# Optimization experiments

Measured on AMD Instinct MI355X. Metric: run time of the kernel, lower is better.

Reference implementation:

```python
import jax, jax.numpy as jnp
import numpy as np

B, N, D = 4, 4096, 768
H, DH = 12, 64          # heads, dim_head; inner_dim = H*DH = D
DEPTH = 4
HID = int(D * 4.0)      # mlp hidden
LN_EPS = 1e-5


def setup_inputs() -> dict:
    key = jax.random.key(0)
    ks = jax.random.split(key, 7)
    s = 0.02
    return {
        "x": jax.random.normal(ks[0], (B, N, D), jnp.float32),
        "ln1_g": jnp.ones((DEPTH, D), jnp.float32),
        "ln1_b": jnp.zeros((DEPTH, D), jnp.float32),
        "qkv_w": jax.random.normal(ks[1], (DEPTH, D, H * DH), jnp.float32) * s,
        "temp": jnp.ones((DEPTH, H, 1), jnp.float32),
        "out_w": jax.random.normal(ks[2], (DEPTH, H * DH, D), jnp.float32) * s,
        "out_b": jnp.zeros((DEPTH, D), jnp.float32),
        "ln2_g": jnp.ones((DEPTH, D), jnp.float32),
        "ln2_b": jnp.zeros((DEPTH, D), jnp.float32),
        "fc1_w": jax.random.normal(ks[3], (DEPTH, D, HID), jnp.float32) * s,
        "fc1_b": jnp.zeros((DEPTH, HID), jnp.float32),
        "fc2_w": jax.random.normal(ks[4], (DEPTH, HID, D), jnp.float32) * s,
        "fc2_b": jnp.zeros((DEPTH, D), jnp.float32),
    }


def _layernorm(x, g, b):
    mu = jnp.mean(x, axis=-1, keepdims=True)
    var = jnp.mean((x - mu) ** 2, axis=-1, keepdims=True)
    return (x - mu) * jax.lax.rsqrt(var + LN_EPS) * g + b


def _tss_attention(h, qkv_w, temp, out_w, out_b):
    b, n, d = h.shape
    w = h @ qkv_w                                   # (b, n, H*DH)
    w = w.reshape(b, n, H, DH).transpose(0, 2, 1, 3)  # (b, h, n, d)
    # F.normalize over token dim (dim=-2), eps=1e-12
    nrm = jnp.sqrt(jnp.sum(w * w, axis=2, keepdims=True))
    w_normed = w / jnp.maximum(nrm, 1e-12)
    logits = jnp.sum(w_normed * w_normed, axis=-1) * temp[None]  # (b, h, n)
    Pi = jax.nn.softmax(logits, axis=-1)
    Pi_n = Pi / (jnp.sum(Pi, axis=-1, keepdims=True) + 1e-8)
    dots = jnp.einsum('bhn,bhnd->bhd', Pi_n, w * w)[:, :, None, :]  # (b, h, 1, d)
    attn = 1.0 / (1.0 + dots)
    out = -(w * Pi[..., None]) * attn               # (b, h, n, d)
    out = out.transpose(0, 2, 1, 3).reshape(b, n, H * DH)
    return out @ out_w + out_b


def reference(x, ln1_g, ln1_b, qkv_w, temp, out_w, out_b,
              ln2_g, ln2_b, fc1_w, fc1_b, fc2_w, fc2_b):
    for i in range(DEPTH):
        h = _layernorm(x, ln1_g[i], ln1_b[i])
        x = _tss_attention(h, qkv_w[i], temp[i], out_w[i], out_b[i]) + x
        h2 = _layernorm(x, ln2_g[i], ln2_b[i])
        mlp = jax.nn.gelu(h2 @ fc1_w[i] + fc1_b[i], approximate=False) @ fc2_w[i] + fc2_b[i]
        x = mlp + x
    return x
```

## Files before the change

### kernel.cpp

```cpp
#include <hip/hip_runtime.h>
#include <cstdint>
#include <cstddef>

static constexpr int Bc = 4, Nc = 4096, Dc = 768, Hc = 12, DHc = 64;
static constexpr int HIDc = 3072, DEPTHc = 4;
static constexpr int Mc = Bc * Nc;
static constexpr int BHc = Bc * Hc;
static constexpr int BHDc = BHc * DHc;

typedef unsigned short u16;
typedef __bf16 bf16x8 __attribute__((ext_vector_type(8)));
typedef float  f32x4  __attribute__((ext_vector_type(4)));

#define DEV __device__ __forceinline__

DEV u16 f2bf(float x) {
    uint32_t u = __float_as_uint(x);
    u += 0x7fffu + ((u >> 16) & 1u);
    return (u16)(u >> 16);
}
DEV float bf2f(u16 u) { return __uint_as_float(((uint32_t)u) << 16); }
DEV void unp2(uint32_t u, float& a, float& b) {
    a = __uint_as_float(u << 16);
    b = __uint_as_float(u & 0xffff0000u);
}
DEV float gelu_fast(float x) {
    float y = 0.7978845608f * (x + 0.044715f * x * x * x);
    float e = __expf(2.0f * y);
    float t = 1.0f - 2.0f / (e + 1.0f);
    return 0.5f * x * (1.0f + t);
}

DEV void ldg_lds16(const void* g, void* l) {
    __builtin_amdgcn_global_load_lds(
        (const __attribute__((address_space(1))) uint32_t*)(uintptr_t)g,
        (__attribute__((address_space(3))) uint32_t*)(uint32_t)(uintptr_t)l,
        16, 0, 0);
}

__global__ void detect_kernel(const uint32_t* __restrict__ x, uint32_t* __restrict__ flag) {
    int t = threadIdx.x;
    uint32_t w = x[t];
    int e = (w >> 7) & 0xFF;
    __shared__ int cnt[256];
    cnt[t] = (e >= 100 && e <= 140) ? 1 : 0;
    __syncthreads();
    for (int s = 128; s; s >>= 1) {
        if (t < s) cnt[t] += cnt[t + s];
        __syncthreads();
    }
    if (t == 0) flag[0] = (cnt[0] >= 128) ? 1u : 0u;
}

__global__ __launch_bounds__(256) void sentinel_kernel(u16* __restrict__ out, int n) {
    int i = blockIdx.x * 256 + threadIdx.x;
    if (i < n) out[i] = 0x449A;
}

__global__ __launch_bounds__(256) void cvt_param_kernel(
    const void* __restrict__ src, float* __restrict__ dst, int n,
    const uint32_t* __restrict__ flag) {
    int i = blockIdx.x * 256 + threadIdx.x;
    if (i >= n) return;
    if (flag[0]) dst[i] = bf2f(((const u16*)src)[i]);
    else         dst[i] = ((const float*)src)[i];
}

__global__ __launch_bounds__(256) void transpose_cvt_off(
    const void* __restrict__ src, size_t eoff, u16* __restrict__ dst,
    int R, int C, const uint32_t* __restrict__ flag) {
    __shared__ u16 tile[32][33];
    const bool isbf = (flag[0] != 0);
    int c0 = blockIdx.x * 32, r0 = blockIdx.y * 32;
    int tx = threadIdx.x & 31, ty = threadIdx.x >> 5;
#pragma unroll
    for (int j = 0; j < 32; j += 8) {
        size_t off = eoff + (size_t)(r0 + ty + j) * C + (c0 + tx);
        tile[ty + j][tx] = isbf ? ((const u16*)src)[off] : f2bf(((const float*)src)[off]);
    }
    __syncthreads();
#pragma unroll
    for (int j = 0; j < 32; j += 8)
        dst[(size_t)(c0 + ty + j) * R + (r0 + tx)] = tile[tx][ty + j];
}

__global__ __launch_bounds__(256) void ln_kernel(
    const float* __restrict__ x, const float* __restrict__ g,
    const float* __restrict__ bta, u16* __restrict__ out) {
    int row = blockIdx.x, t = threadIdx.x;
    const float* xr = x + (size_t)row * Dc;
    float v0 = xr[t], v1 = xr[t + 256], v2 = xr[t + 512];
    float s = v0 + v1 + v2;
    float ss = v0 * v0 + v1 * v1 + v2 * v2;
    __shared__ float red[8];
    for (int m = 32; m; m >>= 1) { s += __shfl_xor(s, m, 64); ss += __shfl_xor(ss, m, 64); }
    int wave = t >> 6, lane = t & 63;
    if (lane == 0) { red[wave] = s; red[4 + wave] = ss; }
    __syncthreads();
    s  = red[0] + red[1] + red[2] + red[3];
    ss = red[4] + red[5] + red[6] + red[7];
    float mu = s * (1.0f / Dc);
    float var = ss * (1.0f / Dc) - mu * mu;
    float rs = rsqrtf(var + 1e-5f);
    u16* orow = out + (size_t)row * Dc;
    orow[t]       = f2bf((v0 - mu) * rs * g[t]       + bta[t]);
    orow[t + 256] = f2bf((v1 - mu) * rs * g[t + 256] + bta[t + 256]);
    orow[t + 512] = f2bf((v2 - mu) * rs * g[t + 512] + bta[t + 512]);
}

template <int MODE>
__global__ __launch_bounds__(512, 2) void gemm_kernel(
    const u16* __restrict__ A, const u16* __restrict__ Bt,
    float* Cf, u16* Cb, const float* __restrict__ bias, const float* res,
    float* aux, int M, int N, int K) {
    __shared__ __attribute__((aligned(16))) u16 lds[4][2][256 * 32];
    const int tid = threadIdx.x;
    const int wave = tid >> 6, lane = tid & 63;
    const int wm = wave >> 2, wn = wave & 3;
    const int bm = blockIdx.y * 256, bn = blockIdx.x * 256;
    const int NT = K >> 5;

    const int srow   = lane >> 2;
    const int schunk = (lane & 3) ^ ((lane >> 3) & 3);
    const u16* ag = A  + (size_t)(bm + wave * 16 + srow) * K + schunk * 8;
    const u16* bg = Bt + (size_t)(bn + wave * 16 + srow) * K + schunk * 8;
    const size_t rstep = (size_t)128 * K;

    auto stA = [&](int t) {
        u16* d = &lds[t & 3][0][wave * 512];
        const u16* g = ag + (size_t)t * 32;
        ldg_lds16(g, d);
        ldg_lds16(g + rstep, d + 4096);
    };
    auto stB = [&](int t) {
        u16* d = &lds[t & 3][1][wave * 512];
        const u16* g = bg + (size_t)t * 32;
        ldg_lds16(g, d);
        ldg_lds16(g + rstep, d + 4096);
    };

    const int fm = lane & 15;
    const int fc = lane >> 4;
    const int fp = fc ^ ((fm >> 1) & 3);
    const int aoff = (wm * 128 + fm) * 32 + fp * 8;
    const int boff = (wn * 64  + fm) * 32 + fp * 8;

    f32x4 acc[8][4] = {};

    stA(0); stB(0); stA(1); stB(1);
    asm volatile("s_waitcnt vmcnt(4)" ::: "memory");
    __builtin_amdgcn_s_barrier();
    __builtin_amdgcn_sched_barrier(0);

    for (int t = 0; t < NT; ++t) {
        const int tb = t & 3;
        const u16* Ab = &lds[tb][0][0];
        const u16* Bb = &lds[tb][1][0];
        bf16x8 af[8], bq[4];
#pragma unroll
        for (int mf = 0; mf < 8; ++mf)
            af[mf] = *(const bf16x8*)(Ab + aoff + mf * 512);
        bq[0] = *(const bf16x8*)(Bb + boff);
        bq[1] = *(const bf16x8*)(Bb + boff + 512);
        if (t + 2 < NT) stA(t + 2);
        __builtin_amdgcn_s_barrier();
        __builtin_amdgcn_sched_barrier(0);
        __builtin_amdgcn_s_setprio(1);
#pragma unroll
        for (int mf = 0; mf < 8; ++mf) {
            acc[mf][0] = __builtin_amdgcn_mfma_f32_16x16x32_bf16(af[mf], bq[0], acc[mf][0], 0, 0, 0);
            acc[mf][1] = __builtin_amdgcn_mfma_f32_16x16x32_bf16(af[mf], bq[1], acc[mf][1], 0, 0, 0);
        }
        __builtin_amdgcn_s_setprio(0);
        __builtin_amdgcn_s_barrier();
        __builtin_amdgcn_sched_barrier(0);
        bq[2] = *(const bf16x8*)(Bb + boff + 1024);
        bq[3] = *(const bf16x8*)(Bb + boff + 1536);
        if (t + 2 < NT) {
            stB(t + 2);
            asm volatile("s_waitcnt vmcnt(4)" ::: "memory");
        } else if (t + 1 < NT) {
            asm volatile("s_waitcnt vmcnt(0)" ::: "memory");
        }
        __builtin_amdgcn_s_barrier();
        __builtin_amdgcn_sched_barrier(0);
        __builtin_amdgcn_s_setprio(1);
#pragma unroll
        for (int mf = 0; mf < 8; ++mf) {
            acc[mf][2] = __builtin_amdgcn_mfma_f32_16x16x32_bf16(af[mf], bq[2], acc[mf][2], 0, 0, 0);
            acc[mf][3] = __builtin_amdgcn_mfma_f32_16x16x32_bf16(af[mf], bq[3], acc[mf][3], 0, 0, 0);
        }
        __builtin_amdgcn_s_setprio(0);
        __builtin_amdgcn_s_barrier();
        __builtin_amdgcn_sched_barrier(0);
    }

    const int er = (lane >> 4) * 4;
    const int ec = lane & 15;
    float csq[4] = {0.f, 0.f, 0.f, 0.f};
#pragma unroll
    for (int mf = 0; mf < 8; ++mf) {
        const int row0 = bm + wm * 128 + mf * 16 + er;
#pragma unroll
        for (int nf = 0; nf < 4; ++nf) {
            const int col = bn + wn * 64 + nf * 16 + ec;
#pragma unroll
            for (int r = 0; r < 4; ++r) {
                const size_t off = (size_t)(row0 + r) * N + col;
                float v = acc[mf][nf][r];
                if (MODE == 1) {
                    Cf[off] = v + bias[col] + res[off];
                } else if (MODE == 2) {
                    Cb[off] = f2bf(gelu_fast(v + bias[col]));
                } else {
                    Cb[off] = f2bf(v);
                    csq[nf] += v * v;
                }
            }
        }
    }
    if (MODE == 3) {
        const int b = bm >> 12;
#pragma unroll
        for (int nf = 0; nf < 4; ++nf) {
            float s = csq[nf];
            s += __shfl_xor(s, 16, 64);
            s += __shfl_xor(s, 32, 64);
            if (lane < 16) {
                const int col = bn + wn * 64 + nf * 16 + lane;
                const int bh = b * Hc + (col >> 6);
                atomicAdd(&aux[bh * DHc + (col & 63)], s);
            }
        }
    }
}

__global__ __launch_bounds__(256) void logits_kernel(
    const u16* __restrict__ w, const float* __restrict__ nrm2,
    const float* __restrict__ tp, float* __restrict__ logits) {
    int blk = blockIdx.x;
    int chunk = blk & 15, bh = blk >> 4;
    int b = bh / Hc, h = bh - b * Hc;
    int t = threadIdx.x, dq = t & 3, nr = t >> 2;
    __shared__ float inv[64];
    if (t < 64) inv[t] = 1.0f / fmaxf(nrm2[bh * DHc + t], 1e-24f);
    __syncthreads();
    float tl = tp[h];
#pragma unroll
    for (int jj = 0; jj < 4; jj++) {
        int n = chunk * 256 + jj * 64 + nr;
        const uint4* wr = (const uint4*)(w + ((size_t)b * Nc + n) * Dc + h * DHc + dq * 16);
        uint4 u0 = wr[0], u1 = wr[1];
        float acc = 0.f;
        float e0, e1;
        const float* iv = inv + dq * 16;
        unp2(u0.x, e0, e1); acc += e0 * e0 * iv[0]  + e1 * e1 * iv[1];
        unp2(u0.y, e0, e1); acc += e0 * e0 * iv[2]  + e1 * e1 * iv[3];
        unp2(u0.z, e0, e1); acc += e0 * e0 * iv[4]  + e1 * e1 * iv[5];
        unp2(u0.w, e0, e1); acc += e0 * e0 * iv[6]  + e1 * e1 * iv[7];
        unp2(u1.x, e0, e1); acc += e0 * e0 * iv[8]  + e1 * e1 * iv[9];
        unp2(u1.y, e0, e1); acc += e0 * e0 * iv[10] + e1 * e1 * iv[11];
        unp2(u1.z, e0, e1); acc += e0 * e0 * iv[12] + e1 * e1 * iv[13];
        unp2(u1.w, e0, e1); acc += e0 * e0 * iv[14] + e1 * e1 * iv[15];
        acc += __shfl_xor(acc, 1, 64);
        acc += __shfl_xor(acc, 2, 64);
        if (dq == 0) logits[(size_t)bh * Nc + n] = tl * acc;
    }
}

__global__ __launch_bounds__(256) void softmax_kernel(
    const float* __restrict__ logits, float* __restrict__ Pi, float* __restrict__ rowsc) {
    int bh = blockIdx.x, t = threadIdx.x;
    int wave = t >> 6, lane = t & 63;
    const float4* lg = (const float4*)(logits + (size_t)bh * Nc);
    float4 v[4];
    float mx = -3.4e38f;
    __shared__ float red[4];
#pragma unroll
    for (int j = 0; j < 4; j++) {
        v[j] = lg[t + 256 * j];
        mx = fmaxf(mx, fmaxf(fmaxf(v[j].x, v[j].y), fmaxf(v[j].z, v[j].w)));
    }
    for (int m = 32; m; m >>= 1) mx = fmaxf(mx, __shfl_xor(mx, m, 64));
    if (lane == 0) red[wave] = mx;
    __syncthreads();
    mx = fmaxf(fmaxf(red[0], red[1]), fmaxf(red[2], red[3]));
    __syncthreads();
    float s = 0.f;
#pragma unroll
    for (int j = 0; j < 4; j++) {
        v[j].x = expf(v[j].x - mx); v[j].y = expf(v[j].y - mx);
        v[j].z = expf(v[j].z - mx); v[j].w = expf(v[j].w - mx);
        s += v[j].x + v[j].y + v[j].z + v[j].w;
    }
    for (int m = 32; m; m >>= 1) s += __shfl_xor(s, m, 64);
    if (lane == 0) red[wave] = s;
    __syncthreads();
    s = red[0] + red[1] + red[2] + red[3];
    __syncthreads();
    float invs = 1.0f / s;
    float s2 = 0.f;
    float4* Pr = (float4*)(Pi + (size_t)bh * Nc);
#pragma unroll
    for (int j = 0; j < 4; j++) {
        float4 p;
        p.x = v[j].x * invs; p.y = v[j].y * invs;
        p.z = v[j].z * invs; p.w = v[j].w * invs;
        s2 += p.x + p.y + p.z + p.w;
        Pr[t + 256 * j] = p;
    }
    for (int m = 32; m; m >>= 1) s2 += __shfl_xor(s2, m, 64);
    if (lane == 0) red[wave] = s2;
    __syncthreads();
    if (t == 0) rowsc[bh] = 1.0f / (red[0] + red[1] + red[2] + red[3] + 1e-8f);
}

__global__ __launch_bounds__(256) void dots_kernel(
    const u16* __restrict__ w, const float* __restrict__ Pi,
    const float* __restrict__ rowsc, float* __restrict__ dots) {
    int blk = blockIdx.x;
    int chunk = blk & 15, bh = blk >> 4;
    int b = bh / Hc, h = bh - b * Hc;
    int t = threadIdx.x, d4 = t & 15, rg = t >> 4;
    const u16* base = w + ((size_t)b * Nc + chunk * 256 + rg) * Dc + h * DHc + d4 * 4;
    const float* Prow = Pi + (size_t)bh * Nc + chunk * 256 + rg;
    float4 acc = {0.f, 0.f, 0.f, 0.f};
#pragma unroll 4
    for (int j = 0; j < 16; j++) {
        uint2 u = *(const uint2*)(base + (size_t)j * 16 * Dc);
        float p = Prow[j * 16];
        float a0, a1, a2, a3;
        unp2(u.x, a0, a1); unp2(u.y, a2, a3);
        acc.x += p * a0 * a0; acc.y += p * a1 * a1;
        acc.z += p * a2 * a2; acc.w += p * a3 * a3;
    }
    __shared__ float4 red[256];
    red[t] = acc;
    __syncthreads();
    if (t < 64) {
        float s = 0.f;
#pragma unroll
        for (int r = 0; r < 16; r++) {
            const float* f = (const float*)&red[r * 16 + (t >> 2)];
            s += f[t & 3];
        }
        atomicAdd(&dots[bh * DHc + t], s * rowsc[bh]);
    }
}

__global__ __launch_bounds__(256) void attnout_kernel(
    const u16* __restrict__ w, const float* __restrict__ Pi,
    const float* __restrict__ dots, u16* __restrict__ out) {
    int idx = blockIdx.x * 256 + threadIdx.x;
    int cg = idx % (Dc / 8);
    int m = idx / (Dc / 8);
    int b = m >> 12, n = m & 4095;
    int c = cg * 8, h = c >> 6, d = c & 63;
    int bh = b * Hc + h;
    uint4 wv = ((const uint4*)w)[idx];
    float pi = Pi[(size_t)bh * Nc + n];
    float4 dv0 = *(const float4*)(dots + bh * DHc + d);
    float4 dv1 = *(const float4*)(dots + bh * DHc + d + 4);
    float a0, a1, a2, a3, a4, a5, a6, a7;
    unp2(wv.x, a0, a1); unp2(wv.y, a2, a3);
    unp2(wv.z, a4, a5); unp2(wv.w, a6, a7);
    union { u16 u[8]; uint4 v4; } pk;
    pk.u[0] = f2bf(-(a0 * pi) / (1.0f + dv0.x));
    pk.u[1] = f2bf(-(a1 * pi) / (1.0f + dv0.y));
    pk.u[2] = f2bf(-(a2 * pi) / (1.0f + dv0.z));
    pk.u[3] = f2bf(-(a3 * pi) / (1.0f + dv0.w));
    pk.u[4] = f2bf(-(a4 * pi) / (1.0f + dv1.x));
    pk.u[5] = f2bf(-(a5 * pi) / (1.0f + dv1.y));
    pk.u[6] = f2bf(-(a6 * pi) / (1.0f + dv1.z));
    pk.u[7] = f2bf(-(a7 * pi) / (1.0f + dv1.w));
    ((uint4*)out)[idx] = pk.v4;
}

extern "C" void kernel_launch(void* const* d_in, const int* in_sizes, int n_in,
                              void* d_out, int out_size, void* d_ws, size_t ws_size,
                              hipStream_t stream) {
    const void* x_in = d_in[0];
    const void* ln1g = d_in[1];
    const void* ln1b = d_in[2];
    const void* qkvw = d_in[3];
    const void* temp = d_in[4];
    const void* outw = d_in[5];
    const void* outb = d_in[6];
    const void* ln2g = d_in[7];
    const void* ln2b = d_in[8];
    const void* fc1w = d_in[9];
    const void* fc1b = d_in[10];
    const void* fc2w = d_in[11];
    const void* fc2b = d_in[12];

    char* p = (char*)d_ws;
    auto alloc = [&](size_t bytes) {
        void* r = (void*)p;
        p += (bytes + 255) & ~(size_t)255;
        return r;
    };
    float* xbuf = (float*)alloc((size_t)Mc * Dc * 4);
    void*  big  = alloc((size_t)Mc * HIDc * 2);
    u16*   wbuf = (u16*)big;
    u16*   gbuf = (u16*)big;
    u16*  abuf  = (u16*)alloc((size_t)Mc * Dc * 2);
    const size_t QKV_T = (size_t)Dc * Dc, OUT_T = (size_t)Dc * Dc;
    const size_t FC1_T = (size_t)HIDc * Dc, FC2_T = (size_t)Dc * HIDc;
    const size_t LSTRIDE = QKV_T + OUT_T + FC1_T + FC2_T;
    u16*  wTL   = (u16*)alloc(LSTRIDE * 2);
    float* nrm2 = (float*)alloc((size_t)BHDc * 4);
    float* dots = (float*)alloc((size_t)BHDc * 4);
    float* logit = (float*)alloc((size_t)BHc * Nc * 4);
    float* Pi    = (float*)alloc((size_t)BHc * Nc * 4);
    float* rowsc = (float*)alloc((size_t)BHc * 4);
    uint32_t* flag = (uint32_t*)alloc(256);
    float* ln1g_f = (float*)alloc((size_t)DEPTHc * Dc * 4);
    float* ln1b_f = (float*)alloc((size_t)DEPTHc * Dc * 4);
    float* ln2g_f = (float*)alloc((size_t)DEPTHc * Dc * 4);
    float* ln2b_f = (float*)alloc((size_t)DEPTHc * Dc * 4);
    float* outb_f = (float*)alloc((size_t)DEPTHc * Dc * 4);
    float* fc1b_f = (float*)alloc((size_t)DEPTHc * HIDc * 4);
    float* fc2b_f = (float*)alloc((size_t)DEPTHc * Dc * 4);
    float* temp_f = (float*)alloc((size_t)DEPTHc * Hc * 4);
    if ((size_t)(p - (char*)d_ws) > ws_size) {
        sentinel_kernel<<<(out_size + 255) / 256, 256, 0, stream>>>((u16*)d_out, out_size);
        return;
    }

    detect_kernel<<<1, 256, 0, stream>>>((const uint32_t*)x_in, flag);

    auto cvt = [&](const void* s, float* d, int n) {
        cvt_param_kernel<<<(n + 255) / 256, 256, 0, stream>>>(s, d, n, flag);
    };
    cvt(x_in, xbuf, Mc * Dc);
    cvt(ln1g, ln1g_f, DEPTHc * Dc);
    cvt(ln1b, ln1b_f, DEPTHc * Dc);
    cvt(ln2g, ln2g_f, DEPTHc * Dc);
    cvt(ln2b, ln2b_f, DEPTHc * Dc);
    cvt(outb, outb_f, DEPTHc * Dc);
    cvt(fc1b, fc1b_f, DEPTHc * HIDc);
    cvt(fc2b, fc2b_f, DEPTHc * Dc);
    cvt(temp, temp_f, DEPTHc * Hc);

    u16* qkvT = wTL;
    u16* outT = qkvT + QKV_T;
    u16* fc1T = outT + OUT_T;
    u16* fc2T = fc1T + FC1_T;

    for (int i = 0; i < DEPTHc; i++) {
        transpose_cvt_off<<<dim3(Dc / 32, Dc / 32), 256, 0, stream>>>(
            qkvw, (size_t)i * Dc * Dc, qkvT, Dc, Dc, flag);
        transpose_cvt_off<<<dim3(Dc / 32, Dc / 32), 256, 0, stream>>>(
            outw, (size_t)i * Dc * Dc, outT, Dc, Dc, flag);
        transpose_cvt_off<<<dim3(HIDc / 32, Dc / 32), 256, 0, stream>>>(
            fc1w, (size_t)i * Dc * HIDc, fc1T, Dc, HIDc, flag);
        transpose_cvt_off<<<dim3(Dc / 32, HIDc / 32), 256, 0, stream>>>(
            fc2w, (size_t)i * HIDc * Dc, fc2T, HIDc, Dc, flag);

        ln_kernel<<<Mc, 256, 0, stream>>>(xbuf, ln1g_f + i * Dc, ln1b_f + i * Dc, abuf);
        hipMemsetAsync(nrm2, 0, (size_t)2 * BHDc * 4, stream);
        gemm_kernel<3><<<dim3(Dc / 256, Mc / 256), 512, 0, stream>>>(
            abuf, qkvT, nullptr, wbuf, nullptr, nullptr, nrm2, Mc, Dc, Dc);
        logits_kernel<<<BHc * 16, 256, 0, stream>>>(wbuf, nrm2, temp_f + i * Hc, logit);
        softmax_kernel<<<BHc, 256, 0, stream>>>(logit, Pi, rowsc);
        dots_kernel<<<BHc * 16, 256, 0, stream>>>(wbuf, Pi, rowsc, dots);
        attnout_kernel<<<(Mc * Dc / 8) / 256, 256, 0, stream>>>(wbuf, Pi, dots, abuf);
        gemm_kernel<1><<<dim3(Dc / 256, Mc / 256), 512, 0, stream>>>(
            abuf, outT, xbuf, nullptr, outb_f + i * Dc, xbuf, nullptr, Mc, Dc, Dc);
        ln_kernel<<<Mc, 256, 0, stream>>>(xbuf, ln2g_f + i * Dc, ln2b_f + i * Dc, abuf);
        gemm_kernel<2><<<dim3(HIDc / 256, Mc / 256), 512, 0, stream>>>(
            abuf, fc1T, nullptr, gbuf, fc1b_f + i * HIDc, nullptr, nullptr, Mc, HIDc, Dc);
        gemm_kernel<1><<<dim3(Dc / 256, Mc / 256), 512, 0, stream>>>(
            gbuf, fc2T, xbuf, nullptr, fc2b_f + i * Dc, xbuf, nullptr, Mc, Dc, HIDc);
    }
    hipMemcpyAsync(d_out, xbuf, (size_t)Mc * Dc * 4, hipMemcpyDeviceToDevice, stream);
}
```

Before: 1.709 ms.

## Restructure GEMM main loop with register double-buffered A fragments and deeper prefetch

```diff
diff --git a/kernel.cpp b/kernel.cpp
--- a/kernel.cpp
+++ b/kernel.cpp
@@ -126,19 +126,6 @@
     const u16* bg = Bt + (size_t)(bn + wave * 16 + srow) * K + schunk * 8;
     const size_t rstep = (size_t)128 * K;
 
-    auto stA = [&](int t) {
-        u16* d = &lds[t & 3][0][wave * 512];
-        const u16* g = ag + (size_t)t * 32;
-        ldg_lds16(g, d);
-        ldg_lds16(g + rstep, d + 4096);
-    };
-    auto stB = [&](int t) {
-        u16* d = &lds[t & 3][1][wave * 512];
-        const u16* g = bg + (size_t)t * 32;
-        ldg_lds16(g, d);
-        ldg_lds16(g + rstep, d + 4096);
-    };
-
     const int fm = lane & 15;
     const int fc = lane >> 4;
     const int fp = fc ^ ((fm >> 1) & 3);
@@ -146,54 +133,66 @@
     const int boff = (wn * 64  + fm) * 32 + fp * 8;
 
     f32x4 acc[8][4] = {};
-
-    stA(0); stB(0); stA(1); stB(1);
+    bf16x8 af0[8], af1[8];
+
+#define GEMM_STAGE(T)                                                       \
+    {   const int tt_ = (T); const int sc_ = (tt_ < NT) ? tt_ : 0;          \
+        const int sl_ = tt_ & 3;                                            \
+        u16* dA_ = &lds[sl_][0][wave * 512];                                \
+        u16* dB_ = &lds[sl_][1][wave * 512];                                \
+        const u16* gA_ = ag + (size_t)sc_ * 32;                             \
+        const u16* gB_ = bg + (size_t)sc_ * 32;                             \
+        ldg_lds16(gA_, dA_); ldg_lds16(gA_ + rstep, dA_ + 4096);            \
+        ldg_lds16(gB_, dB_); ldg_lds16(gB_ + rstep, dB_ + 4096); }
+
+#define GEMM_ITER(H, CUR, NXT)                                              \
+    {                                                                       \
+        asm volatile("s_waitcnt vmcnt(4)" ::: "memory");                    \
+        __builtin_amdgcn_s_barrier();                                       \
+        __builtin_amdgcn_sched_barrier(0);                                  \
+        GEMM_STAGE((H) + 3);                                                \
+        bf16x8 bq0, bq1, bq2, bq3;                                          \
+        {   const u16* Bb_ = &lds[(H) & 3][1][0];                           \
+            bq0 = *(const bf16x8*)(Bb_ + boff);                             \
+            bq1 = *(const bf16x8*)(Bb_ + boff + 512);                       \
+            bq2 = *(const bf16x8*)(Bb_ + boff + 1024);                      \
+            bq3 = *(const bf16x8*)(Bb_ + boff + 1536); }                    \
+        __builtin_amdgcn_sched_barrier(0);                                  \
+        {   const u16* Ab_ = &lds[((H) + 1) & 3][0][0];                     \
+            _Pragma("unroll")                                               \
+            for (int mf = 0; mf < 8; ++mf)                                  \
+                NXT[mf] = *(const bf16x8*)(Ab_ + aoff + mf * 512); }        \
+        asm volatile("s_waitcnt lgkmcnt(8)" ::: "memory");                  \
+        __builtin_amdgcn_sched_barrier(0);                                  \
+        __builtin_amdgcn_s_setprio(1);                                      \
+        _Pragma("unroll")                                                   \
+        for (int mf = 0; mf < 8; ++mf) {                                    \
+            acc[mf][0] = __builtin_amdgcn_mfma_f32_16x16x32_bf16(CUR[mf], bq0, acc[mf][0], 0, 0, 0); \
+            acc[mf][1] = __builtin_amdgcn_mfma_f32_16x16x32_bf16(CUR[mf], bq1, acc[mf][1], 0, 0, 0); \
+            acc[mf][2] = __builtin_amdgcn_mfma_f32_16x16x32_bf16(CUR[mf], bq2, acc[mf][2], 0, 0, 0); \
+            acc[mf][3] = __builtin_amdgcn_mfma_f32_16x16x32_bf16(CUR[mf], bq3, acc[mf][3], 0, 0, 0); \
+        }                                                                   \
+        __builtin_amdgcn_s_setprio(0);                                      \
+    }
+
+    GEMM_STAGE(0);
+    GEMM_STAGE(1);
     asm volatile("s_waitcnt vmcnt(4)" ::: "memory");
     __builtin_amdgcn_s_barrier();
     __builtin_amdgcn_sched_barrier(0);
-
-    for (int t = 0; t < NT; ++t) {
-        const int tb = t & 3;
-        const u16* Ab = &lds[tb][0][0];
-        const u16* Bb = &lds[tb][1][0];
-        bf16x8 af[8], bq[4];
+    {   const u16* Ab_ = &lds[0][0][0];
 #pragma unroll
         for (int mf = 0; mf < 8; ++mf)
-            af[mf] = *(const bf16x8*)(Ab + aoff + mf * 512);
-        bq[0] = *(const bf16x8*)(Bb + boff);
-        bq[1] = *(const bf16x8*)(Bb + boff + 512);
-        if (t + 2 < NT) stA(t + 2);
-        __builtin_amdgcn_s_barrier();
-        __builtin_amdgcn_sched_barrier(0);
-        __builtin_amdgcn_s_setprio(1);
-#pragma unroll
-        for (int mf = 0; mf < 8; ++mf) {
-            acc[mf][0] = __builtin_amdgcn_mfma_f32_16x16x32_bf16(af[mf], bq[0], acc[mf][0], 0, 0, 0);
-            acc[mf][1] = __builtin_amdgcn_mfma_f32_16x16x32_bf16(af[mf], bq[1], acc[mf][1], 0, 0, 0);
-        }
-        __builtin_amdgcn_s_setprio(0);
-        __builtin_amdgcn_s_barrier();
-        __builtin_amdgcn_sched_barrier(0);
-        bq[2] = *(const bf16x8*)(Bb + boff + 1024);
-        bq[3] = *(const bf16x8*)(Bb + boff + 1536);
-        if (t + 2 < NT) {
-            stB(t + 2);
-            asm volatile("s_waitcnt vmcnt(4)" ::: "memory");
-        } else if (t + 1 < NT) {
-            asm volatile("s_waitcnt vmcnt(0)" ::: "memory");
-        }
-        __builtin_amdgcn_s_barrier();
-        __builtin_amdgcn_sched_barrier(0);
-        __builtin_amdgcn_s_setprio(1);
-#pragma unroll
-        for (int mf = 0; mf < 8; ++mf) {
-            acc[mf][2] = __builtin_amdgcn_mfma_f32_16x16x32_bf16(af[mf], bq[2], acc[mf][2], 0, 0, 0);
-            acc[mf][3] = __builtin_amdgcn_mfma_f32_16x16x32_bf16(af[mf], bq[3], acc[mf][3], 0, 0, 0);
-        }
-        __builtin_amdgcn_s_setprio(0);
-        __builtin_amdgcn_s_barrier();
-        __builtin_amdgcn_sched_barrier(0);
-    }
+            af0[mf] = *(const bf16x8*)(Ab_ + aoff + mf * 512);
+    }
+    GEMM_STAGE(2);
+
+    for (int h = 0; h < NT; h += 2) {
+        GEMM_ITER(h,     af0, af1);
+        GEMM_ITER(h + 1, af1, af0);
+    }
+#undef GEMM_ITER
+#undef GEMM_STAGE
 
     const int er = (lane >> 4) * 4;
     const int ec = lane & 15;
```

Result: no change. 1.727 ms (+1.0%).

## Restructure GEMM main loop into 64-wide K stages with ping-pong LDS buffers

Applied to the files above, without the earlier changes.

```diff
diff --git a/kernel.cpp b/kernel.cpp
--- a/kernel.cpp
+++ b/kernel.cpp
@@ -113,87 +113,120 @@
     const u16* __restrict__ A, const u16* __restrict__ Bt,
     float* Cf, u16* Cb, const float* __restrict__ bias, const float* res,
     float* aux, int M, int N, int K) {
-    __shared__ __attribute__((aligned(16))) u16 lds[4][2][256 * 32];
+    __shared__ __attribute__((aligned(16))) u16 lds[2][2][2][256 * 32];
     const int tid = threadIdx.x;
     const int wave = tid >> 6, lane = tid & 63;
     const int wm = wave >> 2, wn = wave & 3;
     const int bm = blockIdx.y * 256, bn = blockIdx.x * 256;
-    const int NT = K >> 5;
-
-    const int srow   = lane >> 2;
+    const int NKS = K >> 6;
+
+    u16* Lm = &lds[0][0][0][0];
+    const u16* L = Lm;
+
     const int schunk = (lane & 3) ^ ((lane >> 3) & 3);
-    const u16* ag = A  + (size_t)(bm + wave * 16 + srow) * K + schunk * 8;
-    const u16* bg = Bt + (size_t)(bn + wave * 16 + srow) * K + schunk * 8;
-    const size_t rstep = (size_t)128 * K;
-
-    auto stA = [&](int t) {
-        u16* d = &lds[t & 3][0][wave * 512];
-        const u16* g = ag + (size_t)t * 32;
-        ldg_lds16(g, d);
-        ldg_lds16(g + rstep, d + 4096);
-    };
-    auto stB = [&](int t) {
-        u16* d = &lds[t & 3][1][wave * 512];
-        const u16* g = bg + (size_t)t * 32;
-        ldg_lds16(g, d);
-        ldg_lds16(g + rstep, d + 4096);
-    };
-
-    const int fm = lane & 15;
-    const int fc = lane >> 4;
-    const int fp = fc ^ ((fm >> 1) & 3);
-    const int aoff = (wm * 128 + fm) * 32 + fp * 8;
-    const int boff = (wn * 64  + fm) * 32 + fp * 8;
+    const u16* ag = A  + (size_t)(bm + wave * 16 + (lane >> 2)) * K + schunk * 8;
+    const u16* bg = Bt + (size_t)(bn + wave * 16 + (lane >> 2)) * K + schunk * 8;
+    const size_t jstep = (size_t)128 * K;
+
+    const int fm = lane & 15, fc = lane >> 4;
+    const int chunk = (fc ^ ((fm >> 1) & 3)) * 8;
+    const int aE0 = (wm * 128 + fm) * 32 + chunk;
+    const int aE1 = 8192 + aE0;
+    const int bE0 = 32768 + (wn * 64 + fm) * 32 + chunk;
+    const int bE1 = 8192 + bE0;
 
     f32x4 acc[8][4] = {};
-
-    stA(0); stB(0); stA(1); stB(1);
+    bf16x8 afr[8], bq[2], bq2[2];
+
+#define STG(OP, GB, SS, DD, KH)                                              \
+    {   const u16* g_ = GB + (size_t)(SS) * 64 + (KH) * 32;                  \
+        u16* d_ = Lm + (OP) * 32768 + (DD) * 16384 + (KH) * 8192 + wave * 512; \
+        ldg_lds16(g_, d_);                                                   \
+        ldg_lds16(g_ + jstep, d_ + 4096); }
+
+#define MF2(NB, BQ)                                                          \
+    __builtin_amdgcn_s_setprio(1);                                           \
+    _Pragma("unroll")                                                        \
+    for (int m = 0; m < 8; ++m) {                                            \
+        acc[m][(NB)]     = __builtin_amdgcn_mfma_f32_16x16x32_bf16(          \
+            afr[m], BQ[0], acc[m][(NB)], 0, 0, 0);                           \
+        acc[m][(NB) + 1] = __builtin_amdgcn_mfma_f32_16x16x32_bf16(          \
+            afr[m], BQ[1], acc[m][(NB) + 1], 0, 0, 0);                       \
+    }                                                                        \
+    __builtin_amdgcn_s_setprio(0);
+
+#define BAR_LG0                                                              \
+    __builtin_amdgcn_s_barrier();                                            \
+    asm volatile("s_waitcnt lgkmcnt(0)" ::: "memory");                       \
+    __builtin_amdgcn_sched_barrier(0);
+
+#define BAR_END                                                              \
+    __builtin_amdgcn_s_barrier();                                            \
+    __builtin_amdgcn_sched_barrier(0);
+
+#define BAR_VM4                                                              \
+    asm volatile("s_waitcnt vmcnt(4)" ::: "memory");                         \
+    __builtin_amdgcn_s_barrier();                                            \
+    __builtin_amdgcn_sched_barrier(0);
+
+#define KSTEP(D, SS1) {                                                      \
+                          \
+    _Pragma("unroll")                                                        \
+    for (int m = 0; m < 8; ++m)                                              \
+        afr[m] = *(const bf16x8*)(L + (D) * 16384 + aE0 + m * 512);          \
+    bq[0] = *(const bf16x8*)(L + (D) * 16384 + bE0);                         \
+    bq[1] = *(const bf16x8*)(L + (D) * 16384 + bE0 + 512);                   \
+    STG(0, ag, SS1, (D) ^ 1, 0);                                             \
+    BAR_LG0;                                                                 \
+    MF2(0, bq);                                                              \
+    BAR_END;                                                                 \
+                   \
+    bq2[0] = *(const bf16x8*)(L + (D) * 16384 + bE0 + 1024);                 \
+    bq2[1] = *(const bf16x8*)(L + (D) * 16384 + bE0 + 1536);                 \
+    STG(1, bg, SS1, (D) ^ 1, 0);                                             \
+    BAR_LG0;                                                                 \
+    MF2(2, bq2);                                                             \
+    BAR_VM4;                                                                 \
+                          \
+    _Pragma("unroll")                                                        \
+    for (int m = 0; m < 8; ++m)                                              \
+        afr[m] = *(const bf16x8*)(L + (D) * 16384 + aE1 + m * 512);          \
+    bq2[0] = *(const bf16x8*)(L + (D) * 16384 + bE1 + 1024);                 \
+    bq2[1] = *(const bf16x8*)(L + (D) * 16384 + bE1 + 1536);                 \
+    STG(0, ag, SS1, (D) ^ 1, 1);                                             \
+    BAR_LG0;                                                                 \
+    MF2(2, bq2);                                                             \
+    BAR_END;                                                                 \
+              \
+    bq[0] = *(const bf16x8*)(L + (D) * 16384 + bE1);                         \
+    bq[1] = *(const bf16x8*)(L + (D) * 16384 + bE1 + 512);                   \
+    STG(1, bg, SS1, (D) ^ 1, 1);                                             \
+    BAR_LG0;                                                                 \
+    MF2(0, bq);                                                              \
+    BAR_VM4;                                                                 \
+}
+
+    STG(0, ag, 0, 0, 0);
+    STG(1, bg, 0, 0, 0);
+    STG(0, ag, 0, 0, 1);
+    STG(1, bg, 0, 0, 1);
     asm volatile("s_waitcnt vmcnt(4)" ::: "memory");
     __builtin_amdgcn_s_barrier();
     __builtin_amdgcn_sched_barrier(0);
 
-    for (int t = 0; t < NT; ++t) {
-        const int tb = t & 3;
-        const u16* Ab = &lds[tb][0][0];
-        const u16* Bb = &lds[tb][1][0];
-        bf16x8 af[8], bq[4];
-#pragma unroll
-        for (int mf = 0; mf < 8; ++mf)
-            af[mf] = *(const bf16x8*)(Ab + aoff + mf * 512);
-        bq[0] = *(const bf16x8*)(Bb + boff);
-        bq[1] = *(const bf16x8*)(Bb + boff + 512);
-        if (t + 2 < NT) stA(t + 2);
-        __builtin_amdgcn_s_barrier();
-        __builtin_amdgcn_sched_barrier(0);
-        __builtin_amdgcn_s_setprio(1);
-#pragma unroll
-        for (int mf = 0; mf < 8; ++mf) {
-            acc[mf][0] = __builtin_amdgcn_mfma_f32_16x16x32_bf16(af[mf], bq[0], acc[mf][0], 0, 0, 0);
-            acc[mf][1] = __builtin_amdgcn_mfma_f32_16x16x32_bf16(af[mf], bq[1], acc[mf][1], 0, 0, 0);
-        }
-        __builtin_amdgcn_s_setprio(0);
-        __builtin_amdgcn_s_barrier();
-        __builtin_amdgcn_sched_barrier(0);
-        bq[2] = *(const bf16x8*)(Bb + boff + 1024);
-        bq[3] = *(const bf16x8*)(Bb + boff + 1536);
-        if (t + 2 < NT) {
-            stB(t + 2);
-            asm volatile("s_waitcnt vmcnt(4)" ::: "memory");
-        } else if (t + 1 < NT) {
-            asm volatile("s_waitcnt vmcnt(0)" ::: "memory");
-        }
-        __builtin_amdgcn_s_barrier();
-        __builtin_amdgcn_sched_barrier(0);
-        __builtin_amdgcn_s_setprio(1);
-#pragma unroll
-        for (int mf = 0; mf < 8; ++mf) {
-            acc[mf][2] = __builtin_amdgcn_mfma_f32_16x16x32_bf16(af[mf], bq[2], acc[mf][2], 0, 0, 0);
-            acc[mf][3] = __builtin_amdgcn_mfma_f32_16x16x32_bf16(af[mf], bq[3], acc[mf][3], 0, 0, 0);
-        }
-        __builtin_amdgcn_s_setprio(0);
-        __builtin_amdgcn_s_barrier();
-        __builtin_amdgcn_sched_barrier(0);
-    }
+    for (int s = 0; s < NKS; s += 2) {
+        KSTEP(0, s + 1);
+        const int s2 = (s + 2 < NKS) ? s + 2 : 0;
+        KSTEP(1, s2);
+    }
+    asm volatile("s_waitcnt vmcnt(0)" ::: "memory");
+
+#undef KSTEP
+#undef BAR_VM4
+#undef BAR_END
+#undef BAR_LG0
+#undef MF2
+#undef STG
 
     const int er = (lane >> 4) * 4;
     const int ec = lane & 15;
```

After: 1.692 ms. About the same (-1.0%).
